# Kernel tuning notes

Hardware: AMD Instinct MI355X
Metric: run time of the kernel (lower is better)

Reference implementation:

```python
import jax, jax.numpy as jnp
import numpy as np

B, H, W, D, K = 64, 32, 32, 128, 1024


def setup_inputs() -> dict:
    key = jax.random.key(0)
    k1, k2 = jax.random.split(key)
    z_e = jax.random.normal(k1, (B, H, W, D), dtype=jnp.float32)
    # GlorotUniform over (k, d): limit = sqrt(6 / (k + d))
    limit = float(np.sqrt(6.0 / (K + D)))
    codebook = jax.random.uniform(k2, (K, D), dtype=jnp.float32, minval=-limit, maxval=limit)
    return {"z_e": z_e, "codebook": codebook}


def reference(z_e, codebook):
    # Original: norm = ||z_e[..., None, :] - codebook||_2 over d, then argmin over k.
    # Squared distance has the same argmin; expand to avoid the (B,H,W,k,d) tensor:
    # ||z - c||^2 = ||z||^2 - 2 z.c + ||c||^2
    z2 = jnp.sum(z_e * z_e, axis=-1, keepdims=True)           # (B,H,W,1)
    c2 = jnp.sum(codebook * codebook, axis=-1)                # (k,)
    dots = jnp.einsum('bhwd,kd->bhwk', z_e, codebook)         # (B,H,W,k)
    dist2 = z2 - 2.0 * dots + c2                              # (B,H,W,k)
    q_z = jnp.argmin(dist2, axis=-1)                          # (B,H,W) int
    return q_z
```

## Files before the change

kernel.cpp:

```cpp
#include <hip/hip_runtime.h>
#include <stdint.h>

#define NPTS   65536
#define DDIM   128
#define KCODES 1024

typedef __attribute__((ext_vector_type(8))) _Float16  half8;
typedef __attribute__((ext_vector_type(4))) float     f32x4;
typedef __attribute__((ext_vector_type(4))) int       int4v;
typedef __attribute__((ext_vector_type(2))) _Float16  half2v;

__device__ __forceinline__ void split16(float x, _Float16& hi, _Float16& lo) {
  _Float16 h = (__builtin_fabsf(x) < 6.103515625e-05f) ? (_Float16)0.f : (_Float16)x;
  hi = h;
  lo = (_Float16)(__fmul_rn(__fsub_rn(x, (float)h), 2048.f));
}

__device__ __forceinline__ float np_sumsq_128(const float* __restrict__ row) {
  float r[8];
#pragma unroll
  for (int k = 0; k < 8; ++k) r[k] = __fmul_rn(row[k], row[k]);
  for (int i = 8; i < 128; i += 8)
#pragma unroll
    for (int k = 0; k < 8; ++k) r[k] = __fadd_rn(r[k], __fmul_rn(row[i + k], row[i + k]));
  float s01 = __fadd_rn(r[0], r[1]), s23 = __fadd_rn(r[2], r[3]);
  float s45 = __fadd_rn(r[4], r[5]), s67 = __fadd_rn(r[6], r[7]);
  return __fadd_rn(__fadd_rn(s01, s23), __fadd_rn(s45, s67));
}

__device__ __forceinline__ void async_copy16(const void* g, void* l) {
  auto gp = (const __attribute__((address_space(1))) unsigned int*)(uintptr_t)g;
  auto lp = (__attribute__((address_space(3))) unsigned int*)(unsigned)(uintptr_t)l;
  __builtin_amdgcn_global_load_lds(gp, lp, 16, 0, 0);
}

constexpr size_t SZ_B   = (size_t)KCODES * DDIM * 2;
constexpr size_t OFF_B1 = 0;
constexpr size_t OFF_B2 = SZ_B;
constexpr size_t OFF_C2 = 2 * SZ_B;
constexpr size_t WS_NEED = OFF_C2 + (size_t)KCODES * 4;

__global__ __launch_bounds__(256) void vq_prep_cb(const float* __restrict__ cb,
                                                  _Float16* __restrict__ B1,
                                                  _Float16* __restrict__ B2,
                                                  float* __restrict__ c2) {
  const int w = threadIdx.x >> 6, ln = threadIdx.x & 63;
  const int code = blockIdx.x * 4 + w;
  const float2 cv = ((const float2*)(cb + (size_t)code * DDIM))[ln];
  _Float16 h0, l0, h1, l1;
  split16(cv.x, h0, l0); split16(cv.y, h1, l1);
  const int kg = ln >> 2;
  const int o  = 2 * (ln & 3);
  const size_t dst = (size_t)code * DDIM + (size_t)((kg ^ (code & 15)) * 8 + o);
  *(half2v*)(B1 + dst) = (half2v){h0, h1};
  *(half2v*)(B2 + dst) = (half2v){l0, l1};

  if (threadIdx.x < 32) {
    const int cc = blockIdx.x * 4 + (threadIdx.x >> 3), jj = threadIdx.x & 7;
    const float* row = cb + (size_t)cc * DDIM;
    float e = row[jj];
    float acc = __fmul_rn(e, e);
    for (int i = 1; i < 16; ++i) {
      e = row[i * 8 + jj];
      acc = __fadd_rn(acc, __fmul_rn(e, e));
    }
    float a1 = __fadd_rn(acc, __shfl_xor(acc, 1));
    float a2 = __fadd_rn(a1, __shfl_xor(a1, 2));
    float a4 = __fadd_rn(a2, __shfl_xor(a2, 4));
    if (jj == 0) c2[cc] = a4;
  }
}

__global__ __launch_bounds__(256, 2) void vq_gemm(
    const float* __restrict__ z,
    const unsigned short* __restrict__ B1g, const unsigned short* __restrict__ B2g,
    const float* __restrict__ c2g, int* __restrict__ out) {
  __shared__ alignas(16) char smem[16384 + 16384 + 4096 + 512];
  unsigned short* Bs1 = (unsigned short*)smem;
  unsigned short* Bs2 = (unsigned short*)(smem + 16384);
  float* c2sh = (float*)(smem + 32768);
  float* z2sh = (float*)(smem + 32768 + 4096);
  float* Ls   = (float*)smem;

  const int tid = threadIdx.x;
  const int ln = tid & 63, wr = tid >> 6;
  const int l15 = ln & 15, q = ln >> 4;
  const size_t row0 = (size_t)blockIdx.x * 128;
  const float4* z4 = (const float4*)z;

  for (int cc = 0; cc < 4; ++cc) {
#pragma unroll
    for (int j = 0; j < 4; ++j) {
      const int idx = tid + j * 256;
      float4 v = z4[(row0 + cc * 32) * 32 + idx];
      *(float4*)&Ls[(idx >> 5) * 132 + (idx & 31) * 4] = v;
    }
    __syncthreads();
    {
      const int r = tid >> 3, jj = tid & 7;
      const float* row = &Ls[r * 132];
      float e = row[jj];
      float acc = __fmul_rn(e, e);
      for (int i = 1; i < 16; ++i) {
        e = row[i * 8 + jj];
        acc = __fadd_rn(acc, __fmul_rn(e, e));
      }
      float a1 = __fadd_rn(acc, __shfl_xor(acc, 1));
      float a2 = __fadd_rn(a1, __shfl_xor(a1, 2));
      float a4 = __fadd_rn(a2, __shfl_xor(a2, 4));
      if (jj == 0) z2sh[cc * 32 + r] = a4;
    }
    __syncthreads();
  }

#pragma unroll
  for (int j = 0; j < 4; ++j) {
    const int s = tid + j * 256;
    async_copy16(B2g + s * 8, Bs2 + s * 8);
    async_copy16(B1g + s * 8, Bs1 + s * 8);
  }
  async_copy16(c2g + tid * 4, c2sh + tid * 4);

  half8 a1f[2][4], a2f[2][4];
#pragma unroll
  for (int rf = 0; rf < 2; ++rf) {
    const float* zr = z + (row0 + wr * 32 + rf * 16 + l15) * DDIM;
#pragma unroll
    for (int ks = 0; ks < 4; ++ks) {
      float tmp[8];
      *(float4*)tmp       = *(const float4*)(zr + ks * 32 + q * 8);
      *(float4*)(tmp + 4) = *(const float4*)(zr + ks * 32 + q * 8 + 4);
      half8 h, l;
#pragma unroll
      for (int e = 0; e < 8; ++e) {
        _Float16 hh, ll;
        split16(tmp[e], hh, ll);
        h[e] = hh; l[e] = ll;
      }
      a1f[rf][ks] = h; a2f[rf][ks] = l;
    }
  }

  float mv[8];
  int mi[8];
#pragma unroll
  for (int i = 0; i < 8; ++i) { mv[i] = 3.0e38f; mi[i] = 0; }

  __syncthreads();

  float z2r[8];
#pragma unroll
  for (int rf = 0; rf < 2; ++rf)
#pragma unroll
    for (int reg = 0; reg < 4; ++reg)
      z2r[rf * 4 + reg] = z2sh[wr * 32 + rf * 16 + q * 4 + reg];

  for (int iter = 0; iter < 16; ++iter) {
    const int c0 = iter * 64;
    f32x4 acc[2][4];
#pragma unroll
    for (int rf = 0; rf < 2; ++rf)
#pragma unroll
      for (int cf = 0; cf < 4; ++cf) acc[rf][cf] = (f32x4){0.f, 0.f, 0.f, 0.f};

#pragma unroll
    for (int ks = 0; ks < 4; ++ks) {
      half8 b[4];
#pragma unroll
      for (int cf = 0; cf < 4; ++cf)
        b[cf] = *(const half8*)&Bs2[(cf * 16 + l15) * 128 + (((ks * 4 + q) ^ l15) * 8)];
#pragma unroll
      for (int rf = 0; rf < 2; ++rf)
#pragma unroll
        for (int cf = 0; cf < 4; ++cf)
          acc[rf][cf] = __builtin_amdgcn_mfma_f32_16x16x32_f16(a1f[rf][ks], b[cf],
                                                               acc[rf][cf], 0, 0, 0);
    }

    __syncthreads();
    if (iter < 15) {
#pragma unroll
      for (int j = 0; j < 4; ++j) {
        const int s = tid + j * 256;
        async_copy16(B2g + (size_t)(c0 + 64) * DDIM + s * 8, Bs2 + s * 8);
      }
    }

#pragma unroll
    for (int ks = 0; ks < 4; ++ks) {
      half8 b[4];
#pragma unroll
      for (int cf = 0; cf < 4; ++cf)
        b[cf] = *(const half8*)&Bs1[(cf * 16 + l15) * 128 + (((ks * 4 + q) ^ l15) * 8)];
#pragma unroll
      for (int rf = 0; rf < 2; ++rf)
#pragma unroll
        for (int cf = 0; cf < 4; ++cf)
          acc[rf][cf] = __builtin_amdgcn_mfma_f32_16x16x32_f16(a2f[rf][ks], b[cf],
                                                               acc[rf][cf], 0, 0, 0);
    }
#pragma unroll
    for (int rf = 0; rf < 2; ++rf)
#pragma unroll
      for (int cf = 0; cf < 4; ++cf) acc[rf][cf] = acc[rf][cf] * 4.8828125e-4f;

#pragma unroll
    for (int ks = 0; ks < 4; ++ks) {
      half8 b[4];
#pragma unroll
      for (int cf = 0; cf < 4; ++cf)
        b[cf] = *(const half8*)&Bs1[(cf * 16 + l15) * 128 + (((ks * 4 + q) ^ l15) * 8)];
#pragma unroll
      for (int rf = 0; rf < 2; ++rf)
#pragma unroll
        for (int cf = 0; cf < 4; ++cf)
          acc[rf][cf] = __builtin_amdgcn_mfma_f32_16x16x32_f16(a1f[rf][ks], b[cf],
                                                               acc[rf][cf], 0, 0, 0);
    }

#pragma unroll
    for (int rf = 0; rf < 2; ++rf)
#pragma unroll
      for (int reg = 0; reg < 4; ++reg) {
        const int slot = rf * 4 + reg;
        const float z2v = z2r[slot];
#pragma unroll
        for (int cf = 0; cf < 4; ++cf) {
          const float c2v = c2sh[c0 + cf * 16 + l15];
          float dot = acc[rf][cf][reg];
          float v = __fadd_rn(__fsub_rn(z2v, __fmul_rn(2.f, dot)), c2v);
          int idx = c0 + cf * 16 + l15;
          if (v < mv[slot]) { mv[slot] = v; mi[slot] = idx; }
        }
      }

    __syncthreads();
    if (iter < 15) {
#pragma unroll
      for (int j = 0; j < 4; ++j) {
        const int s = tid + j * 256;
        async_copy16(B1g + (size_t)(c0 + 64) * DDIM + s * 8, Bs1 + s * 8);
      }
    }
  }

#pragma unroll
  for (int slot = 0; slot < 8; ++slot) {
    float v = mv[slot];
    int i = mi[slot];
#pragma unroll
    for (int m = 1; m <= 8; m <<= 1) {
      float ov = __shfl_xor(v, m);
      int oi = __shfl_xor(i, m);
      if (ov < v || (ov == v && oi < i)) { v = ov; i = oi; }
    }
    mv[slot] = v; mi[slot] = i;
  }

  if (l15 == 0) {
#pragma unroll
    for (int rf = 0; rf < 2; ++rf) {
      int4v r = {mi[rf * 4 + 0], mi[rf * 4 + 1], mi[rf * 4 + 2], mi[rf * 4 + 3]};
      *(int4v*)&out[row0 + wr * 32 + rf * 16 + q * 4] = r;
    }
  }
}

__global__ __launch_bounds__(256) void vq_fallback(const float* __restrict__ z,
                                                   const float* __restrict__ cb,
                                                   int* __restrict__ out) {
  __shared__ float zs[DDIM];
  __shared__ float z2s;
  __shared__ float bv[256];
  __shared__ int bi[256];
  const int p = blockIdx.x, tid = threadIdx.x;
  if (tid < DDIM) zs[tid] = z[(size_t)p * DDIM + tid];
  __syncthreads();
  if (tid == 0) z2s = np_sumsq_128(zs);
  __syncthreads();
  const float z2p = z2s;
  float best = 3.0e38f;
  int bidx = 0;
  for (int c = tid; c < KCODES; c += 256) {
    const float* cr = cb + (size_t)c * DDIM;
    double acc = 0.0;
#pragma unroll 8
    for (int d = 0; d < DDIM; ++d) acc += (double)zs[d] * (double)cr[d];
    float dfl = (float)acc;
    float c2k = np_sumsq_128(cr);
    float v = __fadd_rn(__fsub_rn(z2p, __fmul_rn(2.f, dfl)), c2k);
    if (v < best) { best = v; bidx = c; }
  }
  bv[tid] = best; bi[tid] = bidx;
  __syncthreads();
  for (int off = 128; off > 0; off >>= 1) {
    if (tid < off) {
      if (bv[tid + off] < bv[tid] || (bv[tid + off] == bv[tid] && bi[tid + off] < bi[tid])) {
        bv[tid] = bv[tid + off]; bi[tid] = bi[tid + off];
      }
    }
    __syncthreads();
  }
  if (tid == 0) out[p] = bi[0];
}

extern "C" void kernel_launch(void* const* d_in, const int* in_sizes, int n_in,
                              void* d_out, int out_size, void* d_ws, size_t ws_size,
                              hipStream_t stream) {
  (void)in_sizes; (void)n_in; (void)out_size;
  const float* z = (const float*)d_in[0];
  const float* cb = (const float*)d_in[1];
  int* out = (int*)d_out;

  if (d_ws != nullptr && ws_size >= WS_NEED) {
    char* ws = (char*)d_ws;
    _Float16* B1 = (_Float16*)(ws + OFF_B1);
    _Float16* B2 = (_Float16*)(ws + OFF_B2);
    float* c2 = (float*)(ws + OFF_C2);

    vq_prep_cb<<<KCODES / 4, 256, 0, stream>>>(cb, B1, B2, c2);
    vq_gemm<<<NPTS / 128, 256, 0, stream>>>(
        z, (const unsigned short*)(ws + OFF_B1), (const unsigned short*)(ws + OFF_B2),
        c2, out);
  } else {
    vq_fallback<<<NPTS, 256, 0, stream>>>(z, cb, out);
  }
}
```

Measured before the change: 118.5 us.

## Software-pipeline argmin epilogue with next tile MFMAs and double-buffer z staging

Double-buffers the per-tile accumulators so the distance/argmin epilogue for the previous 64-code tile runs after the current tile's first MFMA pass, letting VALU work overlap matrix ops. Loads each Bs1 fragment once and reuses it for both the lo and hi MFMA passes instead of reading shared memory twice. Double-buffers the z-norm staging so the z2 prologue needs one barrier per chunk instead of two, issues the c2 async copy earlier, and uses an fma in the epilogue. This costs more accumulator and B-fragment registers, which could cause spills or lower occupancy at launch bounds (256,2). The fma also changes rounding slightly, which could flip near-tie argmin results.

```diff
diff --git a/kernel.cpp b/kernel.cpp
--- a/kernel.cpp
+++ b/kernel.cpp
@@ -75,12 +75,13 @@
     const float* __restrict__ z,
     const unsigned short* __restrict__ B1g, const unsigned short* __restrict__ B2g,
     const float* __restrict__ c2g, int* __restrict__ out) {
-  __shared__ alignas(16) char smem[16384 + 16384 + 4096 + 512];
+  __shared__ alignas(16) char smem[33792 + 4096 + 512];
   unsigned short* Bs1 = (unsigned short*)smem;
   unsigned short* Bs2 = (unsigned short*)(smem + 16384);
-  float* c2sh = (float*)(smem + 32768);
-  float* z2sh = (float*)(smem + 32768 + 4096);
-  float* Ls   = (float*)smem;
+  float* c2sh = (float*)(smem + 33792);
+  float* z2sh = (float*)(smem + 33792 + 4096);
+  float* LsA  = (float*)smem;
+  float* LsB  = (float*)(smem + 16896);
 
   const int tid = threadIdx.x;
   const int ln = tid & 63, wr = tid >> 6;
@@ -88,30 +89,35 @@
   const size_t row0 = (size_t)blockIdx.x * 128;
   const float4* z4 = (const float4*)z;
 
-  for (int cc = 0; cc < 4; ++cc) {
+  async_copy16(c2g + tid * 4, c2sh + tid * 4);
+
+  auto stagez = [&](int cc, float* Ls) {
 #pragma unroll
     for (int j = 0; j < 4; ++j) {
       const int idx = tid + j * 256;
       float4 v = z4[(row0 + cc * 32) * 32 + idx];
       *(float4*)&Ls[(idx >> 5) * 132 + (idx & 31) * 4] = v;
     }
+  };
+  stagez(0, LsA);
+  for (int cc = 0; cc < 4; ++cc) {
     __syncthreads();
-    {
-      const int r = tid >> 3, jj = tid & 7;
-      const float* row = &Ls[r * 132];
-      float e = row[jj];
-      float acc = __fmul_rn(e, e);
-      for (int i = 1; i < 16; ++i) {
-        e = row[i * 8 + jj];
-        acc = __fadd_rn(acc, __fmul_rn(e, e));
-      }
-      float a1 = __fadd_rn(acc, __shfl_xor(acc, 1));
-      float a2 = __fadd_rn(a1, __shfl_xor(a1, 2));
-      float a4 = __fadd_rn(a2, __shfl_xor(a2, 4));
-      if (jj == 0) z2sh[cc * 32 + r] = a4;
-    }
-    __syncthreads();
-  }
+    if (cc < 3) stagez(cc + 1, (cc & 1) ? LsA : LsB);
+    const float* Ls = (cc & 1) ? LsB : LsA;
+    const int r = tid >> 3, jj = tid & 7;
+    const float* row = &Ls[r * 132];
+    float e = row[jj];
+    float acc = __fmul_rn(e, e);
+    for (int i = 1; i < 16; ++i) {
+      e = row[i * 8 + jj];
+      acc = __fadd_rn(acc, __fmul_rn(e, e));
+    }
+    float a1 = __fadd_rn(acc, __shfl_xor(acc, 1));
+    float a2 = __fadd_rn(a1, __shfl_xor(a1, 2));
+    float a4 = __fadd_rn(a2, __shfl_xor(a2, 4));
+    if (jj == 0) z2sh[cc * 32 + r] = a4;
+  }
+  __syncthreads();
 
 #pragma unroll
   for (int j = 0; j < 4; ++j) {
@@ -119,7 +125,6 @@
     async_copy16(B2g + s * 8, Bs2 + s * 8);
     async_copy16(B1g + s * 8, Bs1 + s * 8);
   }
-  async_copy16(c2g + tid * 4, c2sh + tid * 4);
 
   half8 a1f[2][4], a2f[2][4];
 #pragma unroll
@@ -155,13 +160,34 @@
     for (int reg = 0; reg < 4; ++reg)
       z2r[rf * 4 + reg] = z2sh[wr * 32 + rf * 16 + q * 4 + reg];
 
-  for (int iter = 0; iter < 16; ++iter) {
-    const int c0 = iter * 64;
-    f32x4 acc[2][4];
+  auto epilogue = [&](f32x4 (&a)[2][4], int c0p) {
+    float c2v[4];
+#pragma unroll
+    for (int cf = 0; cf < 4; ++cf) c2v[cf] = c2sh[c0p + cf * 16 + l15];
 #pragma unroll
     for (int rf = 0; rf < 2; ++rf)
 #pragma unroll
-      for (int cf = 0; cf < 4; ++cf) acc[rf][cf] = (f32x4){0.f, 0.f, 0.f, 0.f};
+      for (int reg = 0; reg < 4; ++reg) {
+        const int slot = rf * 4 + reg;
+#pragma unroll
+        for (int cf = 0; cf < 4; ++cf) {
+          float v = __fadd_rn(__builtin_fmaf(-2.f, a[rf][cf][reg], z2r[slot]), c2v[cf]);
+          int idx = c0p + cf * 16 + l15;
+          if (v < mv[slot]) { mv[slot] = v; mi[slot] = idx; }
+        }
+      }
+  };
+
+  f32x4 acc[2][2][4];
+
+#pragma unroll 2
+  for (int it = 0; it < 16; ++it) {
+    const int p = it & 1;
+    const int c0 = it * 64;
+#pragma unroll
+    for (int rf = 0; rf < 2; ++rf)
+#pragma unroll
+      for (int cf = 0; cf < 4; ++cf) acc[p][rf][cf] = (f32x4){0.f, 0.f, 0.f, 0.f};
 
 #pragma unroll
     for (int ks = 0; ks < 4; ++ks) {
@@ -173,12 +199,14 @@
       for (int rf = 0; rf < 2; ++rf)
 #pragma unroll
         for (int cf = 0; cf < 4; ++cf)
-          acc[rf][cf] = __builtin_amdgcn_mfma_f32_16x16x32_f16(a1f[rf][ks], b[cf],
-                                                               acc[rf][cf], 0, 0, 0);
-    }
+          acc[p][rf][cf] = __builtin_amdgcn_mfma_f32_16x16x32_f16(a1f[rf][ks], b[cf],
+                                                                  acc[p][rf][cf], 0, 0, 0);
+    }
+
+    if (it > 0) epilogue(acc[p ^ 1], (it - 1) * 64);
 
     __syncthreads();
-    if (iter < 15) {
+    if (it < 15) {
 #pragma unroll
       for (int j = 0; j < 4; ++j) {
         const int s = tid + j * 256;
@@ -186,56 +214,37 @@
       }
     }
 
+    half8 b1h[4][4];
 #pragma unroll
     for (int ks = 0; ks < 4; ++ks) {
-      half8 b[4];
 #pragma unroll
       for (int cf = 0; cf < 4; ++cf)
-        b[cf] = *(const half8*)&Bs1[(cf * 16 + l15) * 128 + (((ks * 4 + q) ^ l15) * 8)];
+        b1h[ks][cf] =
+            *(const half8*)&Bs1[(cf * 16 + l15) * 128 + (((ks * 4 + q) ^ l15) * 8)];
 #pragma unroll
       for (int rf = 0; rf < 2; ++rf)
 #pragma unroll
         for (int cf = 0; cf < 4; ++cf)
-          acc[rf][cf] = __builtin_amdgcn_mfma_f32_16x16x32_f16(a2f[rf][ks], b[cf],
-                                                               acc[rf][cf], 0, 0, 0);
+          acc[p][rf][cf] = __builtin_amdgcn_mfma_f32_16x16x32_f16(a2f[rf][ks], b1h[ks][cf],
+                                                                  acc[p][rf][cf], 0, 0, 0);
     }
 #pragma unroll
     for (int rf = 0; rf < 2; ++rf)
 #pragma unroll
-      for (int cf = 0; cf < 4; ++cf) acc[rf][cf] = acc[rf][cf] * 4.8828125e-4f;
+      for (int cf = 0; cf < 4; ++cf) acc[p][rf][cf] = acc[p][rf][cf] * 4.8828125e-4f;
 
 #pragma unroll
     for (int ks = 0; ks < 4; ++ks) {
-      half8 b[4];
-#pragma unroll
-      for (int cf = 0; cf < 4; ++cf)
-        b[cf] = *(const half8*)&Bs1[(cf * 16 + l15) * 128 + (((ks * 4 + q) ^ l15) * 8)];
 #pragma unroll
       for (int rf = 0; rf < 2; ++rf)
 #pragma unroll
         for (int cf = 0; cf < 4; ++cf)
-          acc[rf][cf] = __builtin_amdgcn_mfma_f32_16x16x32_f16(a1f[rf][ks], b[cf],
-                                                               acc[rf][cf], 0, 0, 0);
-    }
-
-#pragma unroll
-    for (int rf = 0; rf < 2; ++rf)
-#pragma unroll
-      for (int reg = 0; reg < 4; ++reg) {
-        const int slot = rf * 4 + reg;
-        const float z2v = z2r[slot];
-#pragma unroll
-        for (int cf = 0; cf < 4; ++cf) {
-          const float c2v = c2sh[c0 + cf * 16 + l15];
-          float dot = acc[rf][cf][reg];
-          float v = __fadd_rn(__fsub_rn(z2v, __fmul_rn(2.f, dot)), c2v);
-          int idx = c0 + cf * 16 + l15;
-          if (v < mv[slot]) { mv[slot] = v; mi[slot] = idx; }
-        }
-      }
+          acc[p][rf][cf] = __builtin_amdgcn_mfma_f32_16x16x32_f16(a1f[rf][ks], b1h[ks][cf],
+                                                                  acc[p][rf][cf], 0, 0, 0);
+    }
 
     __syncthreads();
-    if (iter < 15) {
+    if (it < 15) {
 #pragma unroll
       for (int j = 0; j < 4; ++j) {
         const int s = tid + j * 256;
@@ -243,6 +252,8 @@
       }
     }
   }
+
+  epilogue(acc[1], 960);
 
 #pragma unroll
   for (int slot = 0; slot < 8; ++slot) {
```

Result: slower. 127.5 us (+7.5%).

## Split codebook across two blocks per tile and merge packed argmins

Applied to the files above, without the earlier changes.

The GEMM grid gains a second dimension so each block scans only half of the codebook, doubling the block count to fill the GPU. Each half writes its per-point minimum as a packed 64-bit key (order-preserving float bits plus index), and a small merge kernel selects the smaller key. The z-norm staging is double-buffered and the distance uses an FMA. The cost is redundant z loading and splitting per half, extra workspace traffic, and an extra launch; the larger workspace requirement could route to the fallback path if the buffer is too small.

```diff
diff --git a/kernel.cpp b/kernel.cpp
--- a/kernel.cpp
+++ b/kernel.cpp
@@ -7,7 +7,6 @@
 
 typedef __attribute__((ext_vector_type(8))) _Float16  half8;
 typedef __attribute__((ext_vector_type(4))) float     f32x4;
-typedef __attribute__((ext_vector_type(4))) int       int4v;
 typedef __attribute__((ext_vector_type(2))) _Float16  half2v;
 
 __device__ __forceinline__ void split16(float x, _Float16& hi, _Float16& lo) {
@@ -38,7 +37,8 @@
 constexpr size_t OFF_B1 = 0;
 constexpr size_t OFF_B2 = SZ_B;
 constexpr size_t OFF_C2 = 2 * SZ_B;
-constexpr size_t WS_NEED = OFF_C2 + (size_t)KCODES * 4;
+constexpr size_t OFF_PK = OFF_C2 + (size_t)KCODES * 4;
+constexpr size_t WS_NEED = OFF_PK + (size_t)NPTS * 2 * 8;
 
 __global__ __launch_bounds__(256) void vq_prep_cb(const float* __restrict__ cb,
                                                   _Float16* __restrict__ B1,
@@ -74,52 +74,74 @@
 __global__ __launch_bounds__(256, 2) void vq_gemm(
     const float* __restrict__ z,
     const unsigned short* __restrict__ B1g, const unsigned short* __restrict__ B2g,
-    const float* __restrict__ c2g, int* __restrict__ out) {
-  __shared__ alignas(16) char smem[16384 + 16384 + 4096 + 512];
+    const float* __restrict__ c2g, unsigned long long* __restrict__ pk) {
+  __shared__ alignas(16) char smem[38144];
   unsigned short* Bs1 = (unsigned short*)smem;
   unsigned short* Bs2 = (unsigned short*)(smem + 16384);
-  float* c2sh = (float*)(smem + 32768);
-  float* z2sh = (float*)(smem + 32768 + 4096);
-  float* Ls   = (float*)smem;
+  float* c2sh = (float*)(smem + 33792);
+  float* z2sh = (float*)(smem + 37888);
+  float* LsA  = (float*)smem;
+  float* LsB  = (float*)(smem + 16896);
 
   const int tid = threadIdx.x;
   const int ln = tid & 63, wr = tid >> 6;
   const int l15 = ln & 15, q = ln >> 4;
   const size_t row0 = (size_t)blockIdx.x * 128;
+  const int half = blockIdx.y;
+  const int cbase = half * 512;
   const float4* z4 = (const float4*)z;
 
-  for (int cc = 0; cc < 4; ++cc) {
-#pragma unroll
-    for (int j = 0; j < 4; ++j) {
-      const int idx = tid + j * 256;
-      float4 v = z4[(row0 + cc * 32) * 32 + idx];
-      *(float4*)&Ls[(idx >> 5) * 132 + (idx & 31) * 4] = v;
-    }
-    __syncthreads();
-    {
+  async_copy16(c2g + tid * 4, c2sh + tid * 4);
+
+  float z2r[8];
+  {
+    auto stagez = [&](int cc, float* Ls) {
+#pragma unroll
+      for (int j = 0; j < 4; ++j) {
+        const int idx = tid + j * 256;
+        float4 v = z4[(row0 + cc * 32) * 32 + idx];
+        *(float4*)&Ls[(idx >> 5) * 132 + (idx & 31) * 4] = v;
+      }
+    };
+    stagez(0, LsA);
+    for (int cc = 0; cc < 4; ++cc) {
+      __syncthreads();
+      if (cc < 3) stagez(cc + 1, (cc & 1) ? LsA : LsB);
+      const float* Ls = (cc & 1) ? LsB : LsA;
       const int r = tid >> 3, jj = tid & 7;
-      const float* row = &Ls[r * 132];
-      float e = row[jj];
+      const float* rowp = &Ls[r * 132];
+      float e = rowp[jj];
       float acc = __fmul_rn(e, e);
       for (int i = 1; i < 16; ++i) {
-        e = row[i * 8 + jj];
+        e = rowp[i * 8 + jj];
         acc = __fadd_rn(acc, __fmul_rn(e, e));
       }
       float a1 = __fadd_rn(acc, __shfl_xor(acc, 1));
       float a2 = __fadd_rn(a1, __shfl_xor(a1, 2));
       float a4 = __fadd_rn(a2, __shfl_xor(a2, 4));
-      if (jj == 0) z2sh[cc * 32 + r] = a4;
-    }
-    __syncthreads();
-  }
+      if (jj == 0) z2sh[cc & 1 ? 32 + r : r] = a4;
+      __syncthreads();
+      const int myrow = wr * 32 + q * 4;
+#pragma unroll
+      for (int rf = 0; rf < 2; ++rf) {
+        const int rowa = wr * 32 + rf * 16 + q * 4;
+        if (rowa >= cc * 32 && rowa < (cc + 1) * 32) {
+#pragma unroll
+          for (int reg = 0; reg < 4; ++reg)
+            z2r[rf * 4 + reg] = z2sh[(cc & 1 ? 32 : 0) + (rowa - cc * 32) + reg];
+        }
+      }
+      (void)myrow;
+    }
+  }
+  __syncthreads();
 
 #pragma unroll
   for (int j = 0; j < 4; ++j) {
     const int s = tid + j * 256;
-    async_copy16(B2g + s * 8, Bs2 + s * 8);
-    async_copy16(B1g + s * 8, Bs1 + s * 8);
-  }
-  async_copy16(c2g + tid * 4, c2sh + tid * 4);
+    async_copy16(B2g + (size_t)cbase * DDIM + s * 8, Bs2 + s * 8);
+    async_copy16(B1g + (size_t)cbase * DDIM + s * 8, Bs1 + s * 8);
+  }
 
   half8 a1f[2][4], a2f[2][4];
 #pragma unroll
@@ -148,15 +170,8 @@
 
   __syncthreads();
 
-  float z2r[8];
-#pragma unroll
-  for (int rf = 0; rf < 2; ++rf)
-#pragma unroll
-    for (int reg = 0; reg < 4; ++reg)
-      z2r[rf * 4 + reg] = z2sh[wr * 32 + rf * 16 + q * 4 + reg];
-
-  for (int iter = 0; iter < 16; ++iter) {
-    const int c0 = iter * 64;
+  for (int iter = 0; iter < 8; ++iter) {
+    const int c0 = cbase + iter * 64;
     f32x4 acc[2][4];
 #pragma unroll
     for (int rf = 0; rf < 2; ++rf)
@@ -178,7 +193,7 @@
     }
 
     __syncthreads();
-    if (iter < 15) {
+    if (iter < 7) {
 #pragma unroll
       for (int j = 0; j < 4; ++j) {
         const int s = tid + j * 256;
@@ -223,19 +238,17 @@
 #pragma unroll
       for (int reg = 0; reg < 4; ++reg) {
         const int slot = rf * 4 + reg;
-        const float z2v = z2r[slot];
 #pragma unroll
         for (int cf = 0; cf < 4; ++cf) {
           const float c2v = c2sh[c0 + cf * 16 + l15];
-          float dot = acc[rf][cf][reg];
-          float v = __fadd_rn(__fsub_rn(z2v, __fmul_rn(2.f, dot)), c2v);
+          float v = __fadd_rn(__builtin_fmaf(-2.f, acc[rf][cf][reg], z2r[slot]), c2v);
           int idx = c0 + cf * 16 + l15;
           if (v < mv[slot]) { mv[slot] = v; mi[slot] = idx; }
         }
       }
 
     __syncthreads();
-    if (iter < 15) {
+    if (iter < 7) {
 #pragma unroll
       for (int j = 0; j < 4; ++j) {
         const int s = tid + j * 256;
@@ -260,10 +273,24 @@
   if (l15 == 0) {
 #pragma unroll
     for (int rf = 0; rf < 2; ++rf) {
-      int4v r = {mi[rf * 4 + 0], mi[rf * 4 + 1], mi[rf * 4 + 2], mi[rf * 4 + 3]};
-      *(int4v*)&out[row0 + wr * 32 + rf * 16 + q * 4] = r;
-    }
-  }
+#pragma unroll
+      for (int reg = 0; reg < 4; ++reg) {
+        const int row = wr * 32 + rf * 16 + q * 4 + reg;
+        unsigned ub = __float_as_uint(mv[rf * 4 + reg]);
+        ub = (ub & 0x80000000u) ? ~ub : (ub | 0x80000000u);
+        pk[(size_t)half * NPTS + row0 + row] =
+            (((unsigned long long)ub) << 32) | (unsigned)mi[rf * 4 + reg];
+      }
+    }
+  }
+}
+
+__global__ __launch_bounds__(256) void vq_merge(const unsigned long long* __restrict__ pk,
+                                                int* __restrict__ out) {
+  const int t = blockIdx.x * 256 + threadIdx.x;
+  unsigned long long p0 = pk[t], p1 = pk[NPTS + t];
+  unsigned long long m = p0 < p1 ? p0 : p1;
+  out[t] = (int)(unsigned)(m & 0xFFFFFFFFull);
 }
 
 __global__ __launch_bounds__(256) void vq_fallback(const float* __restrict__ z,
@@ -317,11 +344,13 @@
     _Float16* B1 = (_Float16*)(ws + OFF_B1);
     _Float16* B2 = (_Float16*)(ws + OFF_B2);
     float* c2 = (float*)(ws + OFF_C2);
+    unsigned long long* pk = (unsigned long long*)(ws + OFF_PK);
 
     vq_prep_cb<<<KCODES / 4, 256, 0, stream>>>(cb, B1, B2, c2);
-    vq_gemm<<<NPTS / 128, 256, 0, stream>>>(
+    vq_gemm<<<dim3(NPTS / 128, 2), 256, 0, stream>>>(
         z, (const unsigned short*)(ws + OFF_B1), (const unsigned short*)(ws + OFF_B2),
-        c2, out);
+        c2, pk);
+    vq_merge<<<NPTS / 256, 256, 0, stream>>>(pk, out);
   } else {
     vq_fallback<<<NPTS, 256, 0, stream>>>(z, cb, out);
   }
```

New measurement: 129.4 us. +9.2%, slower.
